# Performance work log

Measured on AMD Instinct MI355X. Metric: run time of the kernel, lower is better.

The kernel has to match this reference:

```python
import jax, jax.numpy as jnp
import numpy as np

DIM = 2048
N_HEADS = 16
KV_LORA = 512
NOPE = 128
ROPE = 64
V_DIM = 128
QK_DIM = NOPE + ROPE  # 192
B, S = 2, 2048
ROPE_THETA = 10000.0
ROPE_FACTOR = 40.0
BETA_FAST, BETA_SLOW = 32, 1
ORIG_LEN, MAX_LEN = 4096, 16384
MSCALE_ARG = 1.0
EPS = 1e-6


def _precompute_freqs(seqlen):
    # DeepSeek YaRN-corrected rotary frequencies (interleaved-pair convention).
    d = ROPE
    freqs = 1.0 / (ROPE_THETA ** (np.arange(0, d, 2, dtype=np.float64) / d))
    if MAX_LEN > ORIG_LEN:
        def corr_dim(n_rot):
            return d * np.log(ORIG_LEN / (n_rot * 2 * np.pi)) / (2 * np.log(ROPE_THETA))
        low = max(int(np.floor(corr_dim(BETA_FAST))), 0)
        high = min(int(np.ceil(corr_dim(BETA_SLOW))), d - 1)
        smooth = 1.0 - np.clip((np.arange(d // 2) - low) / max(high - low, 1e-3), 0, 1)
        freqs = freqs / ROPE_FACTOR * (1 - smooth) + freqs * smooth
    t = np.arange(seqlen, dtype=np.float64)
    ang = np.outer(t, freqs)  # [S, d/2]
    return np.cos(ang).astype(np.float32), np.sin(ang).astype(np.float32)


def softmax_scale():
    scale = QK_DIM ** -0.5
    if MAX_LEN > ORIG_LEN:
        m = 0.1 * MSCALE_ARG * float(np.log(ROPE_FACTOR)) + 1.0
        scale = scale * m * m
    return scale


def setup_inputs() -> dict:
    key = jax.random.key(0)
    ks = jax.random.split(key, 6)
    w_std = 0.02
    fc, fs = _precompute_freqs(S)
    return {
        "x": jax.random.normal(ks[0], (B, S, DIM), jnp.float32),
        "wq": jax.random.normal(ks[1], (N_HEADS * QK_DIM, DIM), jnp.float32) * w_std,
        "wkv_a": jax.random.normal(ks[2], (KV_LORA + ROPE, DIM), jnp.float32) * w_std,
        "kv_norm_w": jnp.ones((KV_LORA,), jnp.float32),
        "wkv_b": jax.random.normal(ks[3], (N_HEADS * (NOPE + V_DIM), KV_LORA), jnp.float32) * w_std,
        "wo": jax.random.normal(ks[4], (DIM, N_HEADS * V_DIM), jnp.float32) * w_std,
        "freqs_cos": jnp.asarray(fc),
        "freqs_sin": jnp.asarray(fs),
    }


def _apply_rotary(x, cos, sin):
    # x: [B, S, H, d]; interleaved complex pairs, cos/sin: [S, d/2]
    xr = x.reshape(*x.shape[:-1], -1, 2)
    x_re, x_im = xr[..., 0], xr[..., 1]
    c = cos[None, :, None, :]
    s = sin[None, :, None, :]
    y_re = x_re * c - x_im * s
    y_im = x_re * s + x_im * c
    return jnp.stack((y_re, y_im), axis=-1).reshape(x.shape)


def _rmsnorm(x, w):
    return x * jax.lax.rsqrt(jnp.mean(x * x, axis=-1, keepdims=True) + EPS) * w


def reference(x, wq, wkv_a, kv_norm_w, wkv_b, wo, freqs_cos, freqs_sin):
    b, s, _ = x.shape
    # Q projection (q_lora_rank == 0 path)
    q = (x @ wq.T).reshape(b, s, N_HEADS, QK_DIM)
    q_nope, q_pe = q[..., :NOPE], q[..., NOPE:]
    q_pe = _apply_rotary(q_pe, freqs_cos, freqs_sin)
    # Low-rank KV compression
    kv = x @ wkv_a.T  # [B, S, 512+64]
    kv_c, k_pe = kv[..., :KV_LORA], kv[..., KV_LORA:]
    k_pe = _apply_rotary(k_pe[:, :, None, :], freqs_cos, freqs_sin)  # [B,S,1,64]
    kv_c = _rmsnorm(kv_c, kv_norm_w)
    kvb = (kv_c @ wkv_b.T).reshape(b, s, N_HEADS, NOPE + V_DIM)
    k_nope, v = kvb[..., :NOPE], kvb[..., NOPE:]
    k = jnp.concatenate([k_nope, jnp.broadcast_to(k_pe, (b, s, N_HEADS, ROPE))], axis=-1)
    # Causal attention
    scores = jnp.einsum("bshd,bthd->bhst", q, k) * softmax_scale()
    causal = jnp.tril(jnp.ones((s, s), bool))
    scores = jnp.where(causal[None, None], scores, jnp.float32(-1e30))
    p = jax.nn.softmax(scores, axis=-1)
    out = jnp.einsum("bhst,bthd->bshd", p, v).reshape(b, s, N_HEADS * V_DIM)
    return out @ wo.T
```

## Files before the change

### kernel.cpp

```cpp
#include <hip/hip_runtime.h>
#include <math.h>

#define NH      16
#define D_NOPE  128
#define D_ROPE  64
#define D_QK    192
#define D_V     128
#define KV_LORA 512
#define NB      2
#define SEQ     2048
#define NTOK    (NB*SEQ)
#define QROW    (NH*D_QK)
#define KVBROW  (NH*(D_NOPE+D_V))
#define EPSF    1e-6f

typedef unsigned short u16;
typedef float  floatx4 __attribute__((ext_vector_type(4)));
typedef __bf16 bf16x8  __attribute__((ext_vector_type(8)));
typedef u16    u16x4   __attribute__((ext_vector_type(4)));
typedef u16    u16x8   __attribute__((ext_vector_type(8)));

__device__ __forceinline__ u16 f2bf(float f) {
    unsigned u = __builtin_bit_cast(unsigned, f);
    return (u16)((u + 0x7fffu + ((u >> 16) & 1u)) >> 16);
}

__device__ __forceinline__ void async_copy16(const void* g, void* l) {
    __builtin_amdgcn_global_load_lds(
        (const __attribute__((address_space(1))) unsigned int*)g,
        (__attribute__((address_space(3))) unsigned int*)l,
        16, 0, 0);
}

__global__ __launch_bounds__(256) void cast_bf16(const float* __restrict__ in,
                                                 u16* __restrict__ out) {
    const int i = (blockIdx.x * 256 + threadIdx.x) * 4;
    const float4 v = *(const float4*)&in[i];
    u16x4 o; o[0] = f2bf(v.x); o[1] = f2bf(v.y); o[2] = f2bf(v.z); o[3] = f2bf(v.w);
    *(u16x4*)&out[i] = o;
}

__global__ __launch_bounds__(256) void cast_pad_wkva(const float* __restrict__ in,
                                                     u16* __restrict__ out) {
    const int i = (blockIdx.x * 256 + threadIdx.x) * 4;
    const int r = i >> 11;
    u16x4 o;
    if (r < 576) {
        const float4 v = *(const float4*)&in[i];
        o[0] = f2bf(v.x); o[1] = f2bf(v.y); o[2] = f2bf(v.z); o[3] = f2bf(v.w);
    } else {
        o[0] = 0; o[1] = 0; o[2] = 0; o[3] = 0;
    }
    *(u16x4*)&out[i] = o;
}

template<int MODE>
__global__ __launch_bounds__(256) void gemm_mfma(const u16* __restrict__ A,
                                                 const u16* __restrict__ B,
                                                 void* __restrict__ Cout,
                                                 u16* __restrict__ kbuf,
                                                 u16* __restrict__ vT,
                                                 int M, int N, int K) {
    __shared__ u16 As[128 * 32];
    __shared__ u16 Bs[128 * 32];
    const int tid  = threadIdx.x;
    const int wave = tid >> 6, lane = tid & 63;
    const int m0 = blockIdx.y * 128, n0 = blockIdx.x * 128;
    const int wm = (wave & 1) * 64, wn = (wave >> 1) * 64;

    const int srow = wave * 32 + (lane >> 2);
    const int kch  = (lane & 3) * 8;
    const u16* gA0 = A + (size_t)(m0 + srow) * K + kch;
    const u16* gA1 = gA0 + (size_t)16 * K;
    const u16* gB0 = B + (size_t)(n0 + srow) * K + kch;
    const u16* gB1 = gB0 + (size_t)16 * K;
    u16* lA0 = &As[(wave * 32) * 32];
    u16* lA1 = &As[(wave * 32 + 16) * 32];
    u16* lB0 = &Bs[(wave * 32) * 32];
    u16* lB1 = &Bs[(wave * 32 + 16) * 32];

    floatx4 acc[4][4];
#pragma unroll
    for (int i = 0; i < 4; ++i)
#pragma unroll
        for (int j = 0; j < 4; ++j) acc[i][j] = 0.f;

    const int lrow = lane & 15;
    const int lkh  = (lane >> 4) * 8;

    for (int k0 = 0; k0 < K; k0 += 32) {
        __syncthreads();
        async_copy16(gA0 + k0, lA0);
        async_copy16(gA1 + k0, lA1);
        async_copy16(gB0 + k0, lB0);
        async_copy16(gB1 + k0, lB1);
        __syncthreads();
        bf16x8 a[4], b[4];
#pragma unroll
        for (int mi = 0; mi < 4; ++mi)
            a[mi] = *(const bf16x8*)&As[(wm + mi * 16 + lrow) * 32 + lkh];
#pragma unroll
        for (int ni = 0; ni < 4; ++ni)
            b[ni] = *(const bf16x8*)&Bs[(wn + ni * 16 + lrow) * 32 + lkh];
#pragma unroll
        for (int mi = 0; mi < 4; ++mi)
#pragma unroll
            for (int ni = 0; ni < 4; ++ni)
                acc[mi][ni] = __builtin_amdgcn_mfma_f32_16x16x32_bf16(
                    a[mi], b[ni], acc[mi][ni], 0, 0, 0);
    }

    const int crow = (lane >> 4) * 4, ccol = lane & 15;
#pragma unroll
    for (int mi = 0; mi < 4; ++mi)
#pragma unroll
        for (int ni = 0; ni < 4; ++ni) {
            const int m = m0 + wm + mi * 16 + crow;
            const int c = n0 + wn + ni * 16 + ccol;
            if (MODE == 0) {
                float* cp = (float*)Cout + (size_t)m * N + c;
#pragma unroll
                for (int r = 0; r < 4; ++r) cp[(size_t)r * N] = acc[mi][ni][r];
            } else if (MODE == 1) {
                u16* cp = (u16*)Cout + (size_t)m * N + c;
#pragma unroll
                for (int r = 0; r < 4; ++r) cp[(size_t)r * N] = f2bf(acc[mi][ni][r]);
            } else {
                const int hh = c >> 8, j = c & 255;
                const int bb = m >> 11, t = m & 2047;
                if (j < 128) {
#pragma unroll
                    for (int r = 0; r < 4; ++r)
                        kbuf[(((size_t)hh * 2 + bb) * 2048 + t + r) * 192 + j] =
                            f2bf(acc[mi][ni][r]);
                } else {
                    u16x4 pk;
#pragma unroll
                    for (int r = 0; r < 4; ++r) pk[r] = f2bf(acc[mi][ni][r]);
                    *(u16x4*)&vT[(((size_t)hh * 2 + bb) * 128 + (j - 128)) * 2048 + t] = pk;
                }
            }
        }
}


__global__ __launch_bounds__(256) void kv_fix(const float* __restrict__ kv_raw,
                                              const float* __restrict__ w,
                                              const float* __restrict__ fcos,
                                              const float* __restrict__ fsin,
                                              u16* __restrict__ kvn_bf,
                                              u16* __restrict__ kbuf) {
    const int row = blockIdx.x;
    const int tid = threadIdx.x;
    const float* src = kv_raw + (size_t)row * 640;
    const float v0 = src[tid];
    const float v1 = src[256 + tid];
    float ss = v0 * v0 + v1 * v1;
#pragma unroll
    for (int off = 32; off > 0; off >>= 1) ss += __shfl_down(ss, off, 64);
    __shared__ float red[4];
    __shared__ float kpe_s[64];
    if ((tid & 63) == 0) red[tid >> 6] = ss;
    if (tid < 32) {
        const int s = row & (SEQ - 1);
        const float c  = fcos[s * 32 + tid];
        const float sn = fsin[s * 32 + tid];
        const float xr = src[KV_LORA + 2 * tid];
        const float xi = src[KV_LORA + 2 * tid + 1];
        kpe_s[2 * tid]     = xr * c - xi * sn;
        kpe_s[2 * tid + 1] = xr * sn + xi * c;
    }
    __syncthreads();
    const float tot = red[0] + red[1] + red[2] + red[3];
    const float inv = rsqrtf(tot * (1.0f / KV_LORA) + EPSF);
    kvn_bf[(size_t)row * KV_LORA + tid]       = f2bf(v0 * inv * w[tid]);
    kvn_bf[(size_t)row * KV_LORA + 256 + tid] = f2bf(v1 * inv * w[256 + tid]);
    const int bb = row >> 11, t = row & 2047;
    const int hh = tid >> 4, dg = (tid & 15) * 4;
    u16x4 pk;
#pragma unroll
    for (int j = 0; j < 4; ++j) pk[j] = f2bf(kpe_s[dg + j]);
    *(u16x4*)&kbuf[(((size_t)hh * 2 + bb) * 2048 + t) * 192 + 128 + dg] = pk;
}

__global__ __launch_bounds__(256, 2) void attn_mfma(const u16* __restrict__ qbf,
                                                    const u16* __restrict__ kbuf,
                                                    const u16* __restrict__ vT,
                                                    u16* __restrict__ att,
                                                    float scale) {
    __shared__ __attribute__((aligned(16))) u16 Ks[6 * 64 * 32];
    __shared__ __attribute__((aligned(16))) u16 Vs[2 * 128 * 32];
    __shared__ __attribute__((aligned(16))) u16 Ps[4][32 * 72];
    const int qt = (gridDim.x - 1) - blockIdx.x;
    const int h = blockIdx.y, b = blockIdx.z;
    const int tid = threadIdx.x, wave = tid >> 6, lane = tid & 63;
    const int l15 = lane & 15, lg = lane >> 4;

    int qrow[2];
    bf16x8 qf[2][6];
#pragma unroll
    for (int g = 0; g < 2; ++g) {
        qrow[g] = qt * 128 + g * 64 + wave * 16 + l15;
        const size_t qoff = ((size_t)(b * SEQ + qrow[g])) * QROW + h * 192 + lg * 8;
#pragma unroll
        for (int s = 0; s < 6; ++s) qf[g][s] = *(const bf16x8*)&qbf[qoff + s * 32];
    }

    const u16* kb_base = kbuf + ((size_t)(h * 2 + b)) * 2048 * 192;
    const u16* vt_base = vT   + ((size_t)(h * 2 + b)) * 128 * 2048;

    floatx4 oacc[2][8];
#pragma unroll
    for (int g = 0; g < 2; ++g)
#pragma unroll
        for (int v = 0; v < 8; ++v) oacc[g][v] = 0.f;
    float m_run[2] = {-1e30f, -1e30f}, l_run[2] = {0.f, 0.f};

    const int kt_max = 2 * qt + 1;
    for (int kt = 0; kt <= kt_max; ++kt) {
        const int t0 = kt * 64;
        __syncthreads();
#pragma unroll
        for (int i = 0; i < 6; ++i) {
            const int base = (wave * 6 + i) * 64;
            const int slot = base + lane;
            const int s = slot >> 8, r = slot & 255, tk = r >> 2, ch = r & 3;
            async_copy16(kb_base + ((size_t)(t0 + tk)) * 192 + s * 32 + ch * 8,
                         &Ks[base * 8]);
        }
#pragma unroll
        for (int i = 0; i < 4; ++i) {
            const int base = (wave * 4 + i) * 64;
            const int slot = base + lane;
            const int s = slot >> 9, r = slot & 511, v = r >> 2, ch = r & 3;
            async_copy16(vt_base + ((size_t)v) * 2048 + t0 + s * 32 + ch * 8,
                         &Vs[base * 8]);
        }
        __syncthreads();
        floatx4 sacc[2][4];
#pragma unroll
        for (int g = 0; g < 2; ++g)
#pragma unroll
            for (int mt = 0; mt < 4; ++mt) sacc[g][mt] = 0.f;
#pragma unroll
        for (int s = 0; s < 6; ++s) {
#pragma unroll
            for (int mt = 0; mt < 4; ++mt) {
                const bf16x8 kf = *(const bf16x8*)&Ks[(s * 64 + mt * 16 + l15) * 32 + lg * 8];
#pragma unroll
                for (int g = 0; g < 2; ++g)
                    sacc[g][mt] = __builtin_amdgcn_mfma_f32_16x16x32_bf16(
                        kf, qf[g][s], sacc[g][mt], 0, 0, 0);
            }
        }
        float alpha[2];
#pragma unroll
        for (int g = 0; g < 2; ++g) {
            float p[16];
            float tmax = -1e30f;
#pragma unroll
            for (int mt = 0; mt < 4; ++mt)
#pragma unroll
                for (int r = 0; r < 4; ++r) {
                    const int tglob = t0 + mt * 16 + lg * 4 + r;
                    float v = sacc[g][mt][r] * scale;
                    v = (tglob <= qrow[g]) ? v : -1e30f;
                    p[mt * 4 + r] = v;
                    tmax = fmaxf(tmax, v);
                }
            tmax = fmaxf(tmax, __shfl_xor(tmax, 16));
            tmax = fmaxf(tmax, __shfl_xor(tmax, 32));
            const float mnew = fmaxf(m_run[g], tmax);
            alpha[g] = __expf(m_run[g] - mnew);
            m_run[g] = mnew;
            float rsum = 0.f;
#pragma unroll
            for (int k = 0; k < 16; ++k) { p[k] = __expf(p[k] - mnew); rsum += p[k]; }
            rsum += __shfl_xor(rsum, 16);
            rsum += __shfl_xor(rsum, 32);
            l_run[g] = l_run[g] * alpha[g] + rsum;
#pragma unroll
            for (int mt = 0; mt < 4; ++mt) {
                u16x4 pk;
#pragma unroll
                for (int r = 0; r < 4; ++r) pk[r] = f2bf(p[mt * 4 + r]);
                *(u16x4*)&Ps[wave][(g * 16 + l15) * 72 + mt * 16 + lg * 4] = pk;
            }
        }
#pragma unroll
        for (int g = 0; g < 2; ++g) {
            float af[4];
#pragma unroll
            for (int r = 0; r < 4; ++r) af[r] = __shfl(alpha[g], lg * 4 + r);
#pragma unroll
            for (int vt = 0; vt < 8; ++vt)
#pragma unroll
                for (int r = 0; r < 4; ++r) oacc[g][vt][r] *= af[r];
        }
#pragma unroll
        for (int s = 0; s < 2; ++s) {
            bf16x8 pf[2];
#pragma unroll
            for (int g = 0; g < 2; ++g)
                pf[g] = *(const bf16x8*)&Ps[wave][(g * 16 + l15) * 72 + s * 32 + lg * 8];
#pragma unroll
            for (int vt = 0; vt < 8; ++vt) {
                const bf16x8 vf = *(const bf16x8*)&Vs[(s * 128 + vt * 16 + l15) * 32 + lg * 8];
#pragma unroll
                for (int g = 0; g < 2; ++g)
                    oacc[g][vt] = __builtin_amdgcn_mfma_f32_16x16x32_bf16(
                        pf[g], vf, oacc[g][vt], 0, 0, 0);
            }
        }
    }
#pragma unroll
    for (int g = 0; g < 2; ++g) {
        float lf[4];
#pragma unroll
        for (int r = 0; r < 4; ++r) lf[r] = 1.0f / __shfl(l_run[g], lg * 4 + r);
#pragma unroll
        for (int vt = 0; vt < 8; ++vt)
#pragma unroll
            for (int r = 0; r < 4; ++r) {
                const int orow = b * SEQ + qt * 128 + g * 64 + wave * 16 + lg * 4 + r;
                att[(size_t)orow * 2048 + h * 128 + vt * 16 + l15] =
                    f2bf(oacc[g][vt][r] * lf[r]);
            }
    }
}

extern "C" void kernel_launch(void* const* d_in, const int* in_sizes, int n_in,
                              void* d_out, int out_size, void* d_ws, size_t ws_size,
                              hipStream_t stream) {
    const float* x     = (const float*)d_in[0];
    const float* wq    = (const float*)d_in[1];
    const float* wkv_a = (const float*)d_in[2];
    const float* knw   = (const float*)d_in[3];
    const float* wkv_b = (const float*)d_in[4];
    const float* wo    = (const float*)d_in[5];
    const float* fcos  = (const float*)d_in[6];
    const float* fsin  = (const float*)d_in[7];
    float* out = (float*)d_out;

    char* w = (char*)d_ws;
    u16*   x_bf    = (u16*)w;  w += (size_t)NTOK * 2048 * 2;
    u16*   wq_bf   = (u16*)w;  w += (size_t)QROW * 2048 * 2;
    u16*   wkva_bf = (u16*)w;  w += (size_t)640 * 2048 * 2;
    u16*   wkvb_bf = (u16*)w;  w += (size_t)KVBROW * KV_LORA * 2;
    u16*   wo_bf   = (u16*)w;  w += (size_t)2048 * 2048 * 2;
    u16*   q_bf    = (u16*)w;  w += (size_t)NTOK * QROW * 2;
    float* kv_raw  = (float*)w; w += (size_t)NTOK * 640 * 4;
    u16*   kvn_bf  = (u16*)w;  w += (size_t)NTOK * KV_LORA * 2;
    u16*   kbuf    = (u16*)w;  w += (size_t)NH * NB * SEQ * 192 * 2;
    u16*   vT      = (u16*)w;  w += (size_t)NH * NB * 128 * SEQ * 2;
    u16*   att_bf  = (u16*)w;  w += (size_t)NTOK * 2048 * 2;

    const double mm = 0.1 * 1.0 * log(40.0) + 1.0;
    const float scale = (float)((1.0 / sqrt((double)D_QK)) * mm * mm);

    dim3 blk(256);
    cast_bf16<<<dim3(NTOK * 2048 / 1024), blk, 0, stream>>>(x, x_bf);
    cast_bf16<<<dim3(QROW * 2048 / 1024), blk, 0, stream>>>(wq, wq_bf);
    cast_pad_wkva<<<dim3(640 * 2048 / 1024), blk, 0, stream>>>(wkv_a, wkva_bf);
    cast_bf16<<<dim3(KVBROW * KV_LORA / 1024), blk, 0, stream>>>(wkv_b, wkvb_bf);
    cast_bf16<<<dim3(2048 * 2048 / 1024), blk, 0, stream>>>(wo, wo_bf);
    gemm_mfma<1><<<dim3(QROW / 128, NTOK / 128), blk, 0, stream>>>(
        x_bf, wq_bf, q_bf, nullptr, nullptr, NTOK, QROW, 2048);
    gemm_mfma<0><<<dim3(640 / 128, NTOK / 128), blk, 0, stream>>>(
        x_bf, wkva_bf, kv_raw, nullptr, nullptr, NTOK, 640, 2048);
    kv_fix<<<dim3(NTOK), blk, 0, stream>>>(kv_raw, knw, fcos, fsin, kvn_bf, kbuf);
    gemm_mfma<2><<<dim3(KVBROW / 128, NTOK / 128), blk, 0, stream>>>(
        kvn_bf, wkvb_bf, nullptr, kbuf, vT, NTOK, KVBROW, KV_LORA);
    attn_mfma<<<dim3(SEQ / 128, NH, NB), blk, 0, stream>>>(q_bf, kbuf, vT, att_bf, scale);
    gemm_mfma<0><<<dim3(2048 / 128, NTOK / 128), blk, 0, stream>>>(
        att_bf, wo_bf, out, nullptr, nullptr, NTOK, 2048, 2048);
}
```

Before: 476.0 us.

## Pair causal q-tiles per attention block, skip full-tile masking, merge cast kernels

The attention kernel now launches half as many blocks, and each block handles two query tiles (qt and 15-qt). This balances causal work evenly across blocks instead of relying on reversed launch order. Key tiles that lie entirely below the diagonal skip the per-element causal mask. The five fp32-to-bf16 cast launches are merged into one kernel that picks its source by block range, cutting launch overhead. The risk is that the attention grid drops to 256 blocks of fixed work, which could leave compute units underfilled compared with the dynamic scheduling of 512 uneven blocks.

```diff
diff --git a/kernel.cpp b/kernel.cpp
--- a/kernel.cpp
+++ b/kernel.cpp
@@ -32,26 +32,32 @@
         16, 0, 0);
 }
 
-__global__ __launch_bounds__(256) void cast_bf16(const float* __restrict__ in,
-                                                 u16* __restrict__ out) {
-    const int i = (blockIdx.x * 256 + threadIdx.x) * 4;
-    const float4 v = *(const float4*)&in[i];
-    u16x4 o; o[0] = f2bf(v.x); o[1] = f2bf(v.y); o[2] = f2bf(v.z); o[3] = f2bf(v.w);
-    *(u16x4*)&out[i] = o;
-}
-
-__global__ __launch_bounds__(256) void cast_pad_wkva(const float* __restrict__ in,
-                                                     u16* __restrict__ out) {
-    const int i = (blockIdx.x * 256 + threadIdx.x) * 4;
-    const int r = i >> 11;
+__global__ __launch_bounds__(256) void cast_all(const float* __restrict__ x,
+                                                const float* __restrict__ wq,
+                                                const float* __restrict__ wkva,
+                                                const float* __restrict__ wkvb,
+                                                const float* __restrict__ wo,
+                                                u16* __restrict__ xb,
+                                                u16* __restrict__ wqb,
+                                                u16* __restrict__ wkvab,
+                                                u16* __restrict__ wkvbb,
+                                                u16* __restrict__ wob) {
+    int blk = blockIdx.x;
+    const float* src; u16* dst; bool pad = false;
+    if (blk < 8192)        { src = x;    dst = xb; }
+    else if (blk < 14336)  { blk -= 8192;  src = wq;   dst = wqb; }
+    else if (blk < 15616)  { blk -= 14336; src = wkva; dst = wkvab; pad = true; }
+    else if (blk < 17664)  { blk -= 15616; src = wkvb; dst = wkvbb; }
+    else                   { blk -= 17664; src = wo;   dst = wob; }
+    const int i = (blk * 256 + threadIdx.x) * 4;
     u16x4 o;
-    if (r < 576) {
-        const float4 v = *(const float4*)&in[i];
+    if (pad && (i >> 11) >= 576) {
+        o[0] = 0; o[1] = 0; o[2] = 0; o[3] = 0;
+    } else {
+        const float4 v = *(const float4*)&src[i];
         o[0] = f2bf(v.x); o[1] = f2bf(v.y); o[2] = f2bf(v.z); o[3] = f2bf(v.w);
-    } else {
-        o[0] = 0; o[1] = 0; o[2] = 0; o[3] = 0;
     }
-    *(u16x4*)&out[i] = o;
+    *(u16x4*)&dst[i] = o;
 }
 
 template<int MODE>
@@ -191,141 +197,149 @@
     __shared__ __attribute__((aligned(16))) u16 Ks[6 * 64 * 32];
     __shared__ __attribute__((aligned(16))) u16 Vs[2 * 128 * 32];
     __shared__ __attribute__((aligned(16))) u16 Ps[4][32 * 72];
-    const int qt = (gridDim.x - 1) - blockIdx.x;
+    const int qt0 = blockIdx.x;
     const int h = blockIdx.y, b = blockIdx.z;
     const int tid = threadIdx.x, wave = tid >> 6, lane = tid & 63;
     const int l15 = lane & 15, lg = lane >> 4;
 
-    int qrow[2];
-    bf16x8 qf[2][6];
-#pragma unroll
-    for (int g = 0; g < 2; ++g) {
-        qrow[g] = qt * 128 + g * 64 + wave * 16 + l15;
-        const size_t qoff = ((size_t)(b * SEQ + qrow[g])) * QROW + h * 192 + lg * 8;
-#pragma unroll
-        for (int s = 0; s < 6; ++s) qf[g][s] = *(const bf16x8*)&qbf[qoff + s * 32];
-    }
-
     const u16* kb_base = kbuf + ((size_t)(h * 2 + b)) * 2048 * 192;
     const u16* vt_base = vT   + ((size_t)(h * 2 + b)) * 128 * 2048;
 
-    floatx4 oacc[2][8];
-#pragma unroll
-    for (int g = 0; g < 2; ++g)
-#pragma unroll
-        for (int v = 0; v < 8; ++v) oacc[g][v] = 0.f;
-    float m_run[2] = {-1e30f, -1e30f}, l_run[2] = {0.f, 0.f};
-
-    const int kt_max = 2 * qt + 1;
-    for (int kt = 0; kt <= kt_max; ++kt) {
-        const int t0 = kt * 64;
-        __syncthreads();
-#pragma unroll
-        for (int i = 0; i < 6; ++i) {
-            const int base = (wave * 6 + i) * 64;
-            const int slot = base + lane;
-            const int s = slot >> 8, r = slot & 255, tk = r >> 2, ch = r & 3;
-            async_copy16(kb_base + ((size_t)(t0 + tk)) * 192 + s * 32 + ch * 8,
-                         &Ks[base * 8]);
+    for (int pass = 0; pass < 2; ++pass) {
+        const int qt = pass ? qt0 : (15 - qt0);
+
+        int qrow[2];
+        bf16x8 qf[2][6];
+#pragma unroll
+        for (int g = 0; g < 2; ++g) {
+            qrow[g] = qt * 128 + g * 64 + wave * 16 + l15;
+            const size_t qoff = ((size_t)(b * SEQ + qrow[g])) * QROW + h * 192 + lg * 8;
+#pragma unroll
+            for (int s = 0; s < 6; ++s) qf[g][s] = *(const bf16x8*)&qbf[qoff + s * 32];
         }
-#pragma unroll
-        for (int i = 0; i < 4; ++i) {
-            const int base = (wave * 4 + i) * 64;
-            const int slot = base + lane;
-            const int s = slot >> 9, r = slot & 511, v = r >> 2, ch = r & 3;
-            async_copy16(vt_base + ((size_t)v) * 2048 + t0 + s * 32 + ch * 8,
-                         &Vs[base * 8]);
+
+        floatx4 oacc[2][8];
+#pragma unroll
+        for (int g = 0; g < 2; ++g)
+#pragma unroll
+            for (int v = 0; v < 8; ++v) oacc[g][v] = 0.f;
+        float m_run[2] = {-1e30f, -1e30f}, l_run[2] = {0.f, 0.f};
+
+        const int kt_max = 2 * qt + 1;
+        for (int kt = 0; kt <= kt_max; ++kt) {
+            const int t0 = kt * 64;
+            __syncthreads();
+#pragma unroll
+            for (int i = 0; i < 6; ++i) {
+                const int base = (wave * 6 + i) * 64;
+                const int slot = base + lane;
+                const int s = slot >> 8, r = slot & 255, tk = r >> 2, ch = r & 3;
+                async_copy16(kb_base + ((size_t)(t0 + tk)) * 192 + s * 32 + ch * 8,
+                             &Ks[base * 8]);
+            }
+#pragma unroll
+            for (int i = 0; i < 4; ++i) {
+                const int base = (wave * 4 + i) * 64;
+                const int slot = base + lane;
+                const int s = slot >> 9, r = slot & 511, v = r >> 2, ch = r & 3;
+                async_copy16(vt_base + ((size_t)v) * 2048 + t0 + s * 32 + ch * 8,
+                             &Vs[base * 8]);
+            }
+            __syncthreads();
+            floatx4 sacc[2][4];
+#pragma unroll
+            for (int g = 0; g < 2; ++g)
+#pragma unroll
+                for (int mt = 0; mt < 4; ++mt) sacc[g][mt] = 0.f;
+#pragma unroll
+            for (int s = 0; s < 6; ++s) {
+#pragma unroll
+                for (int mt = 0; mt < 4; ++mt) {
+                    const bf16x8 kf = *(const bf16x8*)&Ks[(s * 64 + mt * 16 + l15) * 32 + lg * 8];
+#pragma unroll
+                    for (int g = 0; g < 2; ++g)
+                        sacc[g][mt] = __builtin_amdgcn_mfma_f32_16x16x32_bf16(
+                            kf, qf[g][s], sacc[g][mt], 0, 0, 0);
+                }
+            }
+            float alpha[2];
+#pragma unroll
+            for (int g = 0; g < 2; ++g) {
+                const bool full = (t0 + 63) <= (qt * 128 + g * 64 + wave * 16);
+                float p[16];
+                float tmax = -1e30f;
+#pragma unroll
+                for (int mt = 0; mt < 4; ++mt)
+#pragma unroll
+                    for (int r = 0; r < 4; ++r) {
+                        float v = sacc[g][mt][r] * scale;
+                        if (!full) {
+                            const int tglob = t0 + mt * 16 + lg * 4 + r;
+                            v = (tglob <= qrow[g]) ? v : -1e30f;
+                        }
+                        p[mt * 4 + r] = v;
+                        tmax = fmaxf(tmax, v);
+                    }
+                tmax = fmaxf(tmax, __shfl_xor(tmax, 16));
+                tmax = fmaxf(tmax, __shfl_xor(tmax, 32));
+                const float mnew = fmaxf(m_run[g], tmax);
+                alpha[g] = __expf(m_run[g] - mnew);
+                m_run[g] = mnew;
+                float rsum = 0.f;
+#pragma unroll
+                for (int k = 0; k < 16; ++k) { p[k] = __expf(p[k] - mnew); rsum += p[k]; }
+                rsum += __shfl_xor(rsum, 16);
+                rsum += __shfl_xor(rsum, 32);
+                l_run[g] = l_run[g] * alpha[g] + rsum;
+#pragma unroll
+                for (int mt = 0; mt < 4; ++mt) {
+                    u16x4 pk;
+#pragma unroll
+                    for (int r = 0; r < 4; ++r) pk[r] = f2bf(p[mt * 4 + r]);
+                    *(u16x4*)&Ps[wave][(g * 16 + l15) * 72 + mt * 16 + lg * 4] = pk;
+                }
+            }
+#pragma unroll
+            for (int g = 0; g < 2; ++g) {
+                float af[4];
+#pragma unroll
+                for (int r = 0; r < 4; ++r) af[r] = __shfl(alpha[g], lg * 4 + r);
+#pragma unroll
+                for (int vt = 0; vt < 8; ++vt)
+#pragma unroll
+                    for (int r = 0; r < 4; ++r) oacc[g][vt][r] *= af[r];
+            }
+#pragma unroll
+            for (int s = 0; s < 2; ++s) {
+                bf16x8 pf[2];
+#pragma unroll
+                for (int g = 0; g < 2; ++g)
+                    pf[g] = *(const bf16x8*)&Ps[wave][(g * 16 + l15) * 72 + s * 32 + lg * 8];
+#pragma unroll
+                for (int vt = 0; vt < 8; ++vt) {
+                    const bf16x8 vf = *(const bf16x8*)&Vs[(s * 128 + vt * 16 + l15) * 32 + lg * 8];
+#pragma unroll
+                    for (int g = 0; g < 2; ++g)
+                        oacc[g][vt] = __builtin_amdgcn_mfma_f32_16x16x32_bf16(
+                            pf[g], vf, oacc[g][vt], 0, 0, 0);
+                }
+            }
+        }
+#pragma unroll
+        for (int g = 0; g < 2; ++g) {
+            float lf[4];
+#pragma unroll
+            for (int r = 0; r < 4; ++r) lf[r] = 1.0f / __shfl(l_run[g], lg * 4 + r);
+#pragma unroll
+            for (int vt = 0; vt < 8; ++vt)
+#pragma unroll
+                for (int r = 0; r < 4; ++r) {
+                    const int orow = b * SEQ + qt * 128 + g * 64 + wave * 16 + lg * 4 + r;
+                    att[(size_t)orow * 2048 + h * 128 + vt * 16 + l15] =
+                        f2bf(oacc[g][vt][r] * lf[r]);
+                }
         }
         __syncthreads();
-        floatx4 sacc[2][4];
-#pragma unroll
-        for (int g = 0; g < 2; ++g)
-#pragma unroll
-            for (int mt = 0; mt < 4; ++mt) sacc[g][mt] = 0.f;
-#pragma unroll
-        for (int s = 0; s < 6; ++s) {
-#pragma unroll
-            for (int mt = 0; mt < 4; ++mt) {
-                const bf16x8 kf = *(const bf16x8*)&Ks[(s * 64 + mt * 16 + l15) * 32 + lg * 8];
-#pragma unroll
-                for (int g = 0; g < 2; ++g)
-                    sacc[g][mt] = __builtin_amdgcn_mfma_f32_16x16x32_bf16(
-                        kf, qf[g][s], sacc[g][mt], 0, 0, 0);
-            }
-        }
-        float alpha[2];
-#pragma unroll
-        for (int g = 0; g < 2; ++g) {
-            float p[16];
-            float tmax = -1e30f;
-#pragma unroll
-            for (int mt = 0; mt < 4; ++mt)
-#pragma unroll
-                for (int r = 0; r < 4; ++r) {
-                    const int tglob = t0 + mt * 16 + lg * 4 + r;
-                    float v = sacc[g][mt][r] * scale;
-                    v = (tglob <= qrow[g]) ? v : -1e30f;
-                    p[mt * 4 + r] = v;
-                    tmax = fmaxf(tmax, v);
-                }
-            tmax = fmaxf(tmax, __shfl_xor(tmax, 16));
-            tmax = fmaxf(tmax, __shfl_xor(tmax, 32));
-            const float mnew = fmaxf(m_run[g], tmax);
-            alpha[g] = __expf(m_run[g] - mnew);
-            m_run[g] = mnew;
-            float rsum = 0.f;
-#pragma unroll
-            for (int k = 0; k < 16; ++k) { p[k] = __expf(p[k] - mnew); rsum += p[k]; }
-            rsum += __shfl_xor(rsum, 16);
-            rsum += __shfl_xor(rsum, 32);
-            l_run[g] = l_run[g] * alpha[g] + rsum;
-#pragma unroll
-            for (int mt = 0; mt < 4; ++mt) {
-                u16x4 pk;
-#pragma unroll
-                for (int r = 0; r < 4; ++r) pk[r] = f2bf(p[mt * 4 + r]);
-                *(u16x4*)&Ps[wave][(g * 16 + l15) * 72 + mt * 16 + lg * 4] = pk;
-            }
-        }
-#pragma unroll
-        for (int g = 0; g < 2; ++g) {
-            float af[4];
-#pragma unroll
-            for (int r = 0; r < 4; ++r) af[r] = __shfl(alpha[g], lg * 4 + r);
-#pragma unroll
-            for (int vt = 0; vt < 8; ++vt)
-#pragma unroll
-                for (int r = 0; r < 4; ++r) oacc[g][vt][r] *= af[r];
-        }
-#pragma unroll
-        for (int s = 0; s < 2; ++s) {
-            bf16x8 pf[2];
-#pragma unroll
-            for (int g = 0; g < 2; ++g)
-                pf[g] = *(const bf16x8*)&Ps[wave][(g * 16 + l15) * 72 + s * 32 + lg * 8];
-#pragma unroll
-            for (int vt = 0; vt < 8; ++vt) {
-                const bf16x8 vf = *(const bf16x8*)&Vs[(s * 128 + vt * 16 + l15) * 32 + lg * 8];
-#pragma unroll
-                for (int g = 0; g < 2; ++g)
-                    oacc[g][vt] = __builtin_amdgcn_mfma_f32_16x16x32_bf16(
-                        pf[g], vf, oacc[g][vt], 0, 0, 0);
-            }
-        }
-    }
-#pragma unroll
-    for (int g = 0; g < 2; ++g) {
-        float lf[4];
-#pragma unroll
-        for (int r = 0; r < 4; ++r) lf[r] = 1.0f / __shfl(l_run[g], lg * 4 + r);
-#pragma unroll
-        for (int vt = 0; vt < 8; ++vt)
-#pragma unroll
-            for (int r = 0; r < 4; ++r) {
-                const int orow = b * SEQ + qt * 128 + g * 64 + wave * 16 + lg * 4 + r;
-                att[(size_t)orow * 2048 + h * 128 + vt * 16 + l15] =
-                    f2bf(oacc[g][vt][r] * lf[r]);
-            }
     }
 }
 
@@ -359,11 +373,8 @@
     const float scale = (float)((1.0 / sqrt((double)D_QK)) * mm * mm);
 
     dim3 blk(256);
-    cast_bf16<<<dim3(NTOK * 2048 / 1024), blk, 0, stream>>>(x, x_bf);
-    cast_bf16<<<dim3(QROW * 2048 / 1024), blk, 0, stream>>>(wq, wq_bf);
-    cast_pad_wkva<<<dim3(640 * 2048 / 1024), blk, 0, stream>>>(wkv_a, wkva_bf);
-    cast_bf16<<<dim3(KVBROW * KV_LORA / 1024), blk, 0, stream>>>(wkv_b, wkvb_bf);
-    cast_bf16<<<dim3(2048 * 2048 / 1024), blk, 0, stream>>>(wo, wo_bf);
+    cast_all<<<dim3(21760), blk, 0, stream>>>(x, wq, wkv_a, wkv_b, wo,
+                                              x_bf, wq_bf, wkva_bf, wkvb_bf, wo_bf);
     gemm_mfma<1><<<dim3(QROW / 128, NTOK / 128), blk, 0, stream>>>(
         x_bf, wq_bf, q_bf, nullptr, nullptr, NTOK, QROW, 2048);
     gemm_mfma<0><<<dim3(640 / 128, NTOK / 128), blk, 0, stream>>>(
@@ -371,7 +382,7 @@
     kv_fix<<<dim3(NTOK), blk, 0, stream>>>(kv_raw, knw, fcos, fsin, kvn_bf, kbuf);
     gemm_mfma<2><<<dim3(KVBROW / 128, NTOK / 128), blk, 0, stream>>>(
         kvn_bf, wkvb_bf, nullptr, kbuf, vT, NTOK, KVBROW, KV_LORA);
-    attn_mfma<<<dim3(SEQ / 128, NH, NB), blk, 0, stream>>>(q_bf, kbuf, vT, att_bf, scale);
+    attn_mfma<<<dim3(SEQ / 256, NH, NB), blk, 0, stream>>>(q_bf, kbuf, vT, att_bf, scale);
     gemm_mfma<0><<<dim3(2048 / 128, NTOK / 128), blk, 0, stream>>>(
         att_bf, wo_bf, out, nullptr, nullptr, NTOK, 2048, 2048);
 }
```

New measurement: 456.3 us. 4.1% less time.
